# Optimization experiments

Measured on AMD Instinct MI355X. Metric: run time of the kernel, lower is better.

Reference implementation:

```python
import jax, jax.numpy as jnp
import numpy as np

N = 100000      # total nodes in batched graph
E_RAND = 1600000  # random edges (avg degree 16); self-loops appended -> E = E_RAND + N
B = 1024        # number of graphs / descriptor batch
DIN, D2D, D3D = 128, 200, 100
DG, DH = 20, 64
H1, H2 = 128, 32
EPS = 1e-5


def _lin_init(key, fan_in, fan_out):
    k1, k2 = jax.random.split(key)
    bound = 1.0 / np.sqrt(fan_in)
    W = jax.random.uniform(k1, (fan_in, fan_out), jnp.float32, -bound, bound)
    b = jax.random.uniform(k2, (fan_out,), jnp.float32, -bound, bound)
    return W, b


def setup_inputs() -> dict:
    key = jax.random.key(0)
    ks = jax.random.split(key, 16)
    feat = jax.random.normal(ks[0], (N, DIN), jnp.float32)
    src_r = jax.random.randint(ks[1], (E_RAND,), 0, N, jnp.int32)
    dst_r = jax.random.randint(ks[2], (E_RAND,), 0, N, jnp.int32)
    loop = jnp.arange(N, dtype=jnp.int32)
    src = jnp.concatenate([src_r, loop])  # self-loops: every node has in-degree >= 1
    dst = jnp.concatenate([dst_r, loop])
    graph_id = ((jnp.arange(N, dtype=jnp.int64) * B) // N).astype(jnp.int32)  # sorted, all B nonempty
    desc_2d = jax.random.normal(ks[3], (B, D2D), jnp.float32)
    desc_3d = jax.random.normal(ks[4], (B, D3D), jnp.float32)
    Wg1, bg1 = _lin_init(ks[5], DIN, 100)
    Wg2, bg2 = _lin_init(ks[6], 100, DG)
    Wpg, bpg = _lin_init(ks[7], DG, DH)
    Wp2, bp2 = _lin_init(ks[8], D2D, DH)
    gain = np.sqrt(6.0 / (DH + DH))
    W2 = jax.random.uniform(ks[9], (DH, DH), jnp.float32, -gain, gain)  # xavier_uniform
    Wf1, bf1 = _lin_init(ks[10], 2 * DH, H1)
    Wf2, bf2 = _lin_init(ks[11], H1, H2)
    Wf3, bf3 = _lin_init(ks[12], H2, 1)
    return dict(feat=feat, src=src, dst=dst, graph_id=graph_id,
                desc_2d=desc_2d, desc_3d=desc_3d,
                Wg1=Wg1, bg1=bg1, Wg2=Wg2, bg2=bg2,
                Wpg=Wpg, bpg=bpg, Wp2=Wp2, bp2=bp2, W2=W2,
                Wf1=Wf1, bf1=bf1, Wf2=Wf2, bf2=bf2, Wf3=Wf3, bf3=bf3,
                bn1_g=jnp.ones((H1,), jnp.float32), bn1_b=jnp.zeros((H1,), jnp.float32),
                bn2_g=jnp.ones((H2,), jnp.float32), bn2_b=jnp.zeros((H2,), jnp.float32))


def _gcn(h, W, b, src, dst):
    # copy_u -> mailbox mean: segment-mean of source feats over destination
    msg = h[src]                                               # [E, d] gather
    s = jax.ops.segment_sum(msg, dst, num_segments=N)          # [N, d]
    deg = jax.ops.segment_sum(jnp.ones((src.shape[0], 1), h.dtype), dst, num_segments=N)
    accum = s / jnp.maximum(deg, 1.0)
    return jax.nn.relu(accum @ W + b)


def _bn(x, g, b):  # BatchNorm1d, training-mode batch stats (biased var)
    mu = jnp.mean(x, axis=0)
    var = jnp.mean(jnp.square(x - mu), axis=0)
    return g * (x - mu) * jax.lax.rsqrt(var + EPS) + b


def reference(feat, src, dst, graph_id, desc_2d, desc_3d,
              Wg1, bg1, Wg2, bg2, Wpg, bpg, Wp2, bp2, W2,
              Wf1, bf1, Wf2, bf2, Wf3, bf3, bn1_g, bn1_b, bn2_g, bn2_b):
    h = _gcn(feat, Wg1, bg1, src, dst)        # relu(GCN1) -> [N,100]
    h = _gcn(h, Wg2, bg2, src, dst)           # relu(GCN2) -> [N,20]
    # dgl.mean_nodes: per-graph mean
    hs = jax.ops.segment_sum(h, graph_id, num_segments=B)
    cnt = jax.ops.segment_sum(jnp.ones((N, 1), h.dtype), graph_id, num_segments=B)
    hg = hs / jnp.maximum(cnt, 1.0)           # [B, 20]
    h_g = hg @ Wpg + bpg                      # [B, 64]
    h_d = desc_2d @ Wp2 + bp2                 # [B, 64]
    gate_vec = jax.nn.sigmoid((h_g @ W2) * h_d)
    v2 = gate_vec * h_d
    fusion = jnp.concatenate([h_g, v2], axis=-1)   # [B, 128]
    out = jax.nn.relu(_bn(fusion @ Wf1 + bf1, bn1_g, bn1_b))
    out = jax.nn.relu(_bn(out @ Wf2 + bf2, bn2_g, bn2_b))
    return out @ Wf3 + bf3                    # [B, 1]
```

## Files before the change

kernel.cpp:

```cpp
#include <hip/hip_runtime.h>
#include <hip/hip_fp8.h>
#include <math.h>

#define N_NODES 100000
#define B_GRAPH 1024
#define NBKT 391
#define NBLK 416
#define CAP 6000

typedef unsigned short ushort_t;
typedef unsigned int uint_t;
typedef unsigned char uchar_t;
typedef __attribute__((ext_vector_type(8))) short short8v;
typedef __attribute__((ext_vector_type(4))) float f32x4;
typedef __attribute__((ext_vector_type(2))) float f32x2;

static inline size_t alignup(size_t x){ return (x + 255) & ~(size_t)255; }

__device__ inline float bflo(uint_t u){
  union{ uint_t i; float f; } v; v.i = u << 16; return v.f;
}
__device__ inline float bfhi(uint_t u){
  union{ uint_t i; float f; } v; v.i = u & 0xffff0000u; return v.f;
}
__device__ inline ushort_t f2bf(float f){
  union{ float f; uint_t i; } v; v.f = f;
  uint_t b = v.i;
  b += 0x7fffu + ((b >> 16) & 1u);
  return (ushort_t)(b >> 16);
}
__device__ inline uint_t packbf(float a, float b){
  return (uint_t)f2bf(a) | ((uint_t)f2bf(b) << 16);
}
__device__ inline uchar_t f2fp8(float f){
  __hip_fp8_e4m3 v(f); return (uchar_t)v.__x;
}

__global__ __launch_bounds__(256) void k_hist(const int* __restrict__ dst,
                                              int* __restrict__ hist_g, int* __restrict__ btot,
                                              int E, int CH){
  __shared__ int h[NBKT];
  int blk = blockIdx.x, t = threadIdx.x;
  for (int i = t; i < NBKT; i += 256) h[i] = 0;
  __syncthreads();
  int s = blk*CH, e = s + CH; if (e > E) e = E;
  for (int i = s + t; i < e; i += 256) atomicAdd(&h[dst[i] >> 8], 1);
  __syncthreads();
  for (int i = t; i < NBKT; i += 256){
    int v = h[i];
    hist_g[i*NBLK + blk] = v;
    if (v) atomicAdd(&btot[i], v);
  }
}

__global__ __launch_bounds__(512) void k_offs(const int* __restrict__ hist_g, const int* __restrict__ btot,
                                              int* __restrict__ offs, int* __restrict__ bbase){
  __shared__ int sc[512];
  int b = blockIdx.x, t = threadIdx.x;
  int acc = 0;
  for (int i = t; i < b; i += 512) acc += btot[i];
  sc[t] = acc; __syncthreads();
  for (int o = 256; o > 0; o >>= 1){ if (t < o) sc[t] += sc[t+o]; __syncthreads(); }
  int bb = sc[0];
  __syncthreads();
  int v = (t < NBLK) ? hist_g[b*NBLK + t] : 0;
  sc[t] = v; __syncthreads();
  for (int off = 1; off < 512; off <<= 1){
    int u = (t >= off) ? sc[t-off] : 0;
    __syncthreads();
    sc[t] += u;
    __syncthreads();
  }
  if (t < NBLK) offs[b*NBLK + t] = bb + sc[t] - v;
  if (t == 0) bbase[b] = bb;
  if (b == NBKT-1 && t == NBLK-1) bbase[NBKT] = bb + sc[t];
}

__global__ __launch_bounds__(256) void k_scatter(const int* __restrict__ src, const int* __restrict__ dst,
                                                 const int* __restrict__ offs, uint_t* __restrict__ pairs,
                                                 int E, int CH){
  __shared__ int base[NBKT];
  int blk = blockIdx.x, t = threadIdx.x;
  for (int i = t; i < NBKT; i += 256) base[i] = offs[i*NBLK + blk];
  __syncthreads();
  int s = blk*CH, e = s + CH; if (e > E) e = E;
  for (int i = s + t; i < e; i += 256){
    int d = dst[i];
    int pos = atomicAdd(&base[d >> 8], 1);
    pairs[pos] = (uint_t)src[i] | ((uint_t)(d & 255) << 17);
  }
}

__global__ __launch_bounds__(256) void k_final(const uint_t* __restrict__ pairs, const int* __restrict__ bbase,
                                               int* __restrict__ rp, int* __restrict__ col){
  __shared__ uint_t buf[CAP];
  __shared__ int dcnt[256];
  __shared__ int sc[256];
  __shared__ int dpos[256];
  int b = blockIdx.x, t = threadIdx.x;
  int s = bbase[b], e = bbase[b+1], n = e - s;
  dcnt[t] = 0;
  const uint_t* P;
  if (n <= CAP){
    for (int i = t; i < n; i += 256) buf[i] = pairs[s + i];
    P = buf;
  } else {
    P = pairs + s;
  }
  __syncthreads();
  for (int i = t; i < n; i += 256) atomicAdd(&dcnt[P[i] >> 17], 1);
  __syncthreads();
  int v = dcnt[t];
  sc[t] = v; __syncthreads();
  for (int off = 1; off < 256; off <<= 1){
    int u = (t >= off) ? sc[t-off] : 0;
    __syncthreads();
    sc[t] += u;
    __syncthreads();
  }
  int ex = sc[t] - v;
  int node = b*256 + t;
  if (node <= N_NODES) rp[node] = s + ex;
  dpos[t] = s + ex;
  __syncthreads();
  for (int i = t; i < n; i += 256){
    uint_t pr = P[i];
    int pos = atomicAdd(&dpos[pr >> 17], 1);
    col[pos] = (int)(pr & 0x1FFFFu);
  }
}

__global__ __launch_bounds__(256) void k_packw(const float* __restrict__ W, ushort_t* __restrict__ wpk){
  int idx = blockIdx.x*256 + threadIdx.x;
  if (idx >= 7*4*64) return;
  int l = idx & 63;
  int s = (idx >> 6) & 3;
  int ct = idx >> 8;
  int colj = ct*16 + (l & 15);
  int kbase = 32*s + ((l >> 4) << 3);
  #pragma unroll
  for (int j = 0; j < 8; j++){
    float w = (colj < 100) ? W[(kbase + j)*100 + colj] : 0.f;
    wpk[idx*8 + j] = f2bf(w);
  }
}

__global__ __launch_bounds__(256) void k_gemm1m(const float* __restrict__ feat, const ushort_t* __restrict__ wpk,
                                                uchar_t* __restrict__ t1, int Nn){
  int wid = threadIdx.x >> 6;
  int lane = threadIdx.x & 63;
  int rt = blockIdx.x*4 + wid;
  int row0 = rt*16;
  if (row0 >= Nn) return;
  short8v a[4];
  const float* arow = feat + (size_t)(row0 + (lane & 15))*128 + ((lane >> 4) << 3);
  #pragma unroll
  for (int s = 0; s < 4; s++){
    float4 f0 = *reinterpret_cast<const float4*>(arow + 32*s);
    float4 f1 = *reinterpret_cast<const float4*>(arow + 32*s + 4);
    union { short8v v; uint_t u[4]; } cv;
    cv.u[0] = packbf(f0.x, f0.y); cv.u[1] = packbf(f0.z, f0.w);
    cv.u[2] = packbf(f1.x, f1.y); cv.u[3] = packbf(f1.z, f1.w);
    a[s] = cv.v;
  }
  const short8v* bfrag = reinterpret_cast<const short8v*>(wpk);
  for (int ct = 0; ct < 7; ct++){
    f32x4 acc = {0.f, 0.f, 0.f, 0.f};
    #pragma unroll
    for (int s = 0; s < 4; s++){
      short8v b = bfrag[(ct*4 + s)*64 + lane];
      acc = __builtin_amdgcn_mfma_f32_16x16x32_bf16(a[s], b, acc, 0, 0, 0);
    }
    int colj = ct*16 + (lane & 15);
    if (colj < 100){
      uchar_t* basep = t1 + colj;
      #pragma unroll
      for (int r = 0; r < 4; r++){
        int row = row0 + ((lane >> 4) << 2) + r;
        basep[(size_t)row*128] = f2fp8(acc[r]);
      }
    }
  }
}

__global__ __launch_bounds__(256) void k_agg1(const uint2* __restrict__ t1q, const int* __restrict__ rp,
                                              const int* __restrict__ col, const float* __restrict__ bias,
                                              uint_t* __restrict__ h1u, int Nn){
  int lane = threadIdx.x & 63;
  int node = blockIdx.x*4 + (threadIdx.x >> 6);
  if (node >= Nn) return;
  int qtr = lane >> 4;
  int q   = lane & 15;
  int rs = rp[node], re = rp[node+1];
  float s0=0.f,s1=0.f,s2=0.f,s3=0.f,s4=0.f,s5=0.f,s6=0.f,s7=0.f;

#if __has_builtin(__builtin_amdgcn_cvt_pk_f32_fp8)
  #define DEC8(U) { \
    f32x2 p0 = __builtin_amdgcn_cvt_pk_f32_fp8((U).x, 0); \
    f32x2 p1 = __builtin_amdgcn_cvt_pk_f32_fp8((U).x, 1); \
    f32x2 p2 = __builtin_amdgcn_cvt_pk_f32_fp8((U).y, 0); \
    f32x2 p3 = __builtin_amdgcn_cvt_pk_f32_fp8((U).y, 1); \
    s0 += p0[0]; s1 += p0[1]; s2 += p1[0]; s3 += p1[1]; \
    s4 += p2[0]; s5 += p2[1]; s6 += p3[0]; s7 += p3[1]; }
#else
  #define F8(B) ({ __hip_fp8_e4m3 _v; _v.__x = (unsigned char)(B); (float)_v; })
  #define DEC8(U) { \
    s0 += F8((U).x); s1 += F8((U).x>>8); s2 += F8((U).x>>16); s3 += F8((U).x>>24); \
    s4 += F8((U).y); s5 += F8((U).y>>8); s6 += F8((U).y>>16); s7 += F8((U).y>>24); }
#endif

  for (int base = rs; base < re; base += 64){
    int idx = base + lane;
    int colv = col[idx < re ? idx : re-1];
    int m = re - base; if (m > 64) m = 64;
    int nq = (m - qtr + 3) >> 2;
    int j = 0;
    for (; j + 4 <= nq; j += 4){
      int c0 = __shfl(colv, 4*(j+0) + qtr);
      int c1 = __shfl(colv, 4*(j+1) + qtr);
      int c2 = __shfl(colv, 4*(j+2) + qtr);
      int c3 = __shfl(colv, 4*(j+3) + qtr);
      uint2 u0 = t1q[(size_t)c0*16 + q];
      uint2 u1 = t1q[(size_t)c1*16 + q];
      uint2 u2 = t1q[(size_t)c2*16 + q];
      uint2 u3 = t1q[(size_t)c3*16 + q];
      DEC8(u0); DEC8(u1); DEC8(u2); DEC8(u3);
    }
    for (; j < nq; j++){
      int c = __shfl(colv, 4*j + qtr);
      uint2 u = t1q[(size_t)c*16 + q];
      DEC8(u);
    }
  }
  s0 += __shfl_xor(s0, 16); s1 += __shfl_xor(s1, 16);
  s2 += __shfl_xor(s2, 16); s3 += __shfl_xor(s3, 16);
  s4 += __shfl_xor(s4, 16); s5 += __shfl_xor(s5, 16);
  s6 += __shfl_xor(s6, 16); s7 += __shfl_xor(s7, 16);
  s0 += __shfl_xor(s0, 32); s1 += __shfl_xor(s1, 32);
  s2 += __shfl_xor(s2, 32); s3 += __shfl_xor(s3, 32);
  s4 += __shfl_xor(s4, 32); s5 += __shfl_xor(s5, 32);
  s6 += __shfl_xor(s6, 32); s7 += __shfl_xor(s7, 32);

  if (lane < 13){
    float inv = 1.f/(float)(re - rs);
    float v[8] = {s0,s1,s2,s3,s4,s5,s6,s7};
    #pragma unroll
    for (int i = 0; i < 8; i++){
      int d = 8*lane + i;
      float bv = bias[d < 100 ? d : 99];
      float x = v[i]*inv + (d < 100 ? bv : 0.f);
      v[i] = x > 0.f ? x : 0.f;
    }
    uint_t p0 = packbf(v[0],v[1]), p1 = packbf(v[2],v[3]);
    uint_t p2 = packbf(v[4],v[5]), p3 = packbf(v[6],v[7]);
    uint_t* o = h1u + (size_t)node*50 + lane*4;
    if (lane < 12){
      uint4 w4; w4.x = p0; w4.y = p1; w4.z = p2; w4.w = p3;
      *reinterpret_cast<uint4*>(o) = w4;
    } else {
      uint2 w2; w2.x = p0; w2.y = p1;
      *reinterpret_cast<uint2*>(o) = w2;
    }
  }
  #undef DEC8
}

__global__ __launch_bounds__(256) void k_gemm2(const uint_t* __restrict__ h1u, const float* __restrict__ W,
                                               ushort_t* __restrict__ t2, int Nn){
  int row = blockIdx.x*256 + threadIdx.x;
  if (row >= Nn) return;
  const uint2* xb = reinterpret_cast<const uint2*>(h1u + (size_t)row*50);
  float acc[20];
  #pragma unroll
  for (int j = 0; j < 20; j++) acc[j] = 0.f;
  #pragma unroll 5
  for (int q = 0; q < 25; q++){
    uint2 u = xb[q];
    float fx = bflo(u.x), fy = bfhi(u.x), fz = bflo(u.y), fw = bfhi(u.y);
    const float* w0 = W + q*80;
    #pragma unroll
    for (int j = 0; j < 20; j++){
      float a = acc[j];
      a = fmaf(fx, w0[j],      a);
      a = fmaf(fy, w0[20 + j], a);
      a = fmaf(fz, w0[40 + j], a);
      a = fmaf(fw, w0[60 + j], a);
      acc[j] = a;
    }
  }
  uint2* o = reinterpret_cast<uint2*>(t2 + (size_t)row*20);
  #pragma unroll
  for (int j = 0; j < 5; j++){
    uint2 v; v.x = packbf(acc[4*j], acc[4*j+1]); v.y = packbf(acc[4*j+2], acc[4*j+3]);
    o[j] = v;
  }
}

__global__ __launch_bounds__(256) void k_agg2(const uint_t* __restrict__ t2u, const int* __restrict__ rp,
                                              const int* __restrict__ col, const float* __restrict__ bias,
                                              float2* __restrict__ h2, int Nn){
  int tid = threadIdx.x;
  int node = blockIdx.x*16 + (tid >> 4);
  int l16 = tid & 15;
  if (node >= Nn) return;
  int rs = rp[node], re = rp[node+1];
  int d2 = l16 < 10 ? l16 : 9;
  int grpb = (tid & 63) & ~15;
  float slo0=0.f, slo1=0.f, shi0=0.f, shi1=0.f;
  for (int base = rs; base < re; base += 16){
    int idx = base + l16;
    int colv = col[idx < re ? idx : re-1];
    int m = re - base; if (m > 16) m = 16;
    int e = 0;
    for (; e + 4 <= m; e += 4){
      int c0 = __shfl(colv, grpb+e+0), c1 = __shfl(colv, grpb+e+1);
      int c2 = __shfl(colv, grpb+e+2), c3 = __shfl(colv, grpb+e+3);
      uint_t u0 = t2u[(size_t)c0*10 + d2];
      uint_t u1 = t2u[(size_t)c1*10 + d2];
      uint_t u2 = t2u[(size_t)c2*10 + d2];
      uint_t u3 = t2u[(size_t)c3*10 + d2];
      slo0 += bflo(u0); shi0 += bfhi(u0);
      slo1 += bflo(u1); shi1 += bfhi(u1);
      slo0 += bflo(u2); shi0 += bfhi(u2);
      slo1 += bflo(u3); shi1 += bfhi(u3);
    }
    for (; e < m; e++){
      int c = __shfl(colv, grpb+e);
      uint_t u = t2u[(size_t)c*10 + d2];
      slo0 += bflo(u); shi0 += bfhi(u);
    }
  }
  if (l16 < 10){
    float inv = 1.f/(float)(re - rs);
    float vlo = (slo0 + slo1)*inv + bias[2*l16];
    float vhi = (shi0 + shi1)*inv + bias[2*l16 + 1];
    vlo = vlo > 0.f ? vlo : 0.f;
    vhi = vhi > 0.f ? vhi : 0.f;
    float2 v; v.x = vlo; v.y = vhi;
    h2[(size_t)node*10 + l16] = v;
  }
}

__global__ __launch_bounds__(256) void k_gmean(const float* __restrict__ h2, float* __restrict__ hg){
  __shared__ float red[240];
  int g = blockIdx.x;
  int t = threadIdx.x;
  int s = (int)(((long long)g      * N_NODES + B_GRAPH - 1) / B_GRAPH);
  int e = (int)(((long long)(g+1)  * N_NODES + B_GRAPH - 1) / B_GRAPH);
  if (t < 240){
    int d  = t % 20;
    int r0 = t / 20;
    float acc = 0.f;
    for (int n = s + r0; n < e; n += 12) acc += h2[(size_t)n*20 + d];
    red[t] = acc;
  }
  __syncthreads();
  if (t < 20){
    float acc = 0.f;
    #pragma unroll
    for (int r = 0; r < 12; r++) acc += red[r*20 + t];
    hg[g*20 + t] = acc / (float)(e - s);
  }
}

__global__ __launch_bounds__(256) void k_headf(const float* __restrict__ hg, const float* __restrict__ Wpg,
                                               const float* __restrict__ bpg, const float* __restrict__ desc2,
                                               const float* __restrict__ Wp2, const float* __restrict__ bp2,
                                               const float* __restrict__ W2, float* __restrict__ fus){
  __shared__ float hGs[4][64];
  int idx = blockIdx.x*256 + threadIdx.x;
  int r = idx >> 6, d = idx & 63;
  int rloc = (threadIdx.x >> 6);
  float a = bpg[d];
  for (int k = 0; k < 20; k++) a = fmaf(hg[r*20 + k], Wpg[k*64 + d], a);
  float hd = bp2[d];
  for (int k = 0; k < 200; k++) hd = fmaf(desc2[r*200 + k], Wp2[k*64 + d], hd);
  hGs[rloc][d] = a;
  __syncthreads();
  float x = 0.f;
  for (int k = 0; k < 64; k++) x = fmaf(hGs[rloc][k], W2[k*64 + d], x);
  float gv = 1.f / (1.f + expf(-x*hd));
  fus[r*128 + d]      = a;
  fus[r*128 + 64 + d] = gv*hd;
}

__global__ __launch_bounds__(256) void k_tr(const float* __restrict__ X, float* __restrict__ XT){
  __shared__ float tile[32][33];
  int rb = blockIdx.x >> 2;
  int cb = blockIdx.x & 3;
  int tx = threadIdx.x & 31;
  int ty = threadIdx.x >> 5;
  #pragma unroll
  for (int i = 0; i < 4; i++){
    int r = rb*32 + ty + 8*i;
    tile[ty + 8*i][tx] = X[(size_t)r*128 + cb*32 + tx];
  }
  __syncthreads();
  #pragma unroll
  for (int i = 0; i < 4; i++){
    int c = cb*32 + ty + 8*i;
    XT[(size_t)c*1024 + rb*32 + tx] = tile[tx][ty + 8*i];
  }
}

__global__ __launch_bounds__(256) void k_bnt(const float* __restrict__ XT, const float* __restrict__ W,
                                             const float* __restrict__ bias, const float* __restrict__ gam,
                                             const float* __restrict__ bet, float* __restrict__ YT,
                                             int Kin, int Jout){
  int j = blockIdx.x;
  int t = threadIdx.x;
  float b0 = bias[j];
  float4 z; z.x = b0; z.y = b0; z.z = b0; z.w = b0;
  for (int k = 0; k < Kin; k++){
    float4 x = reinterpret_cast<const float4*>(XT + (size_t)k*1024)[t];
    float wv = W[k*Jout + j];
    z.x = fmaf(x.x, wv, z.x);
    z.y = fmaf(x.y, wv, z.y);
    z.z = fmaf(x.z, wv, z.z);
    z.w = fmaf(x.w, wv, z.w);
  }
  float s = z.x+z.y+z.z+z.w;
  float q = z.x*z.x+z.y*z.y+z.z*z.z+z.w*z.w;
  __shared__ float rs_[256], rq_[256];
  rs_[t] = s; rq_[t] = q; __syncthreads();
  for (int o = 128; o > 0; o >>= 1){
    if (t < o){ rs_[t] += rs_[t+o]; rq_[t] += rq_[t+o]; }
    __syncthreads();
  }
  float mu  = rs_[0] * (1.f/1024.f);
  float var = rq_[0] * (1.f/1024.f) - mu*mu;
  float inv = 1.f / sqrtf(var + 1e-5f);
  float gj = gam[j], bj = bet[j];
  float4 y;
  y.x = gj*(z.x-mu)*inv + bj; y.x = y.x > 0.f ? y.x : 0.f;
  y.y = gj*(z.y-mu)*inv + bj; y.y = y.y > 0.f ? y.y : 0.f;
  y.z = gj*(z.z-mu)*inv + bj; y.z = y.z > 0.f ? y.z : 0.f;
  y.w = gj*(z.w-mu)*inv + bj; y.w = y.w > 0.f ? y.w : 0.f;
  reinterpret_cast<float4*>(YT + (size_t)j*1024)[t] = y;
}

__global__ __launch_bounds__(256) void k_out(const float* __restrict__ y2T, const float* __restrict__ Wf3,
                                             const float* __restrict__ bf3, float* __restrict__ out){
  int r = blockIdx.x*256 + threadIdx.x;
  if (r >= B_GRAPH) return;
  float a = bf3[0];
  #pragma unroll
  for (int k = 0; k < 32; k++) a = fmaf(y2T[k*1024 + r], Wf3[k], a);
  out[r] = a;
}

extern "C" void kernel_launch(void* const* d_in, const int* in_sizes, int n_in,
                              void* d_out, int out_size, void* d_ws, size_t ws_size,
                              hipStream_t stream){
  const float* feat  = (const float*)d_in[0];
  const int*   src   = (const int*)d_in[1];
  const int*   dst   = (const int*)d_in[2];
  const float* desc2 = (const float*)d_in[4];
  const float* Wg1   = (const float*)d_in[6];
  const float* bg1   = (const float*)d_in[7];
  const float* Wg2   = (const float*)d_in[8];
  const float* bg2   = (const float*)d_in[9];
  const float* Wpg   = (const float*)d_in[10];
  const float* bpg   = (const float*)d_in[11];
  const float* Wp2   = (const float*)d_in[12];
  const float* bp2   = (const float*)d_in[13];
  const float* W2    = (const float*)d_in[14];
  const float* Wf1   = (const float*)d_in[15];
  const float* bf1   = (const float*)d_in[16];
  const float* Wf2   = (const float*)d_in[17];
  const float* bf2   = (const float*)d_in[18];
  const float* Wf3   = (const float*)d_in[19];
  const float* bf3   = (const float*)d_in[20];
  const float* bn1g  = (const float*)d_in[21];
  const float* bn1b  = (const float*)d_in[22];
  const float* bn2g  = (const float*)d_in[23];
  const float* bn2b  = (const float*)d_in[24];
  float* out = (float*)d_out;
  const int E = in_sizes[1];

  char* w = (char*)d_ws;
  int* rp     = (int*)w; w += alignup((size_t)(N_NODES+1)*4);
  int* col    = (int*)w; w += alignup((size_t)E*4);
  int* hist_g = (int*)w; w += alignup((size_t)NBKT*NBLK*4);
  int* offs   = (int*)w; w += alignup((size_t)NBKT*NBLK*4);
  int* btot   = (int*)w; w += alignup((size_t)NBKT*4);
  int* bbase  = (int*)w; w += alignup((size_t)(NBKT+1)*4);
  ushort_t* wpk = (ushort_t*)w; w += alignup((size_t)7*4*64*8*2);
  uchar_t* t1 = (uchar_t*)w; w += alignup((size_t)N_NODES*128);
  char* regionA = w; w += alignup((size_t)N_NODES*50*4);
  ushort_t* t2 = (ushort_t*)w; w += alignup((size_t)N_NODES*20*2);
  float* h2   = (float*)w; w += alignup((size_t)N_NODES*20*4);
  float* hg  = (float*)w; w += alignup((size_t)B_GRAPH*20*4);
  float* fus = (float*)w; w += alignup((size_t)B_GRAPH*128*4);
  float* fusT= (float*)w; w += alignup((size_t)B_GRAPH*128*4);
  float* y1T = (float*)w; w += alignup((size_t)B_GRAPH*128*4);
  float* y2T = (float*)w; w += alignup((size_t)B_GRAPH*32*4);
  uint_t* pairs = (uint_t*)regionA;
  uint_t* h1u   = (uint_t*)regionA;

  const int CH = (E + NBLK - 1)/NBLK;

  hipMemsetAsync(btot, 0, (size_t)NBKT*sizeof(int), stream);
  hipMemsetAsync(t1, 0, (size_t)N_NODES*128, stream);
  k_hist   <<<NBLK, 256, 0, stream>>>(dst, hist_g, btot, E, CH);
  k_offs   <<<NBKT, 512, 0, stream>>>(hist_g, btot, offs, bbase);
  k_scatter<<<NBLK, 256, 0, stream>>>(src, dst, offs, pairs, E, CH);
  k_final  <<<NBKT, 256, 0, stream>>>(pairs, bbase, rp, col);

  k_packw  <<<7, 256, 0, stream>>>(Wg1, wpk);
  k_gemm1m <<<(N_NODES/16 + 3)/4, 256, 0, stream>>>(feat, wpk, t1, N_NODES);
  k_agg1   <<<(N_NODES+3)/4, 256, 0, stream>>>((const uint2*)t1, rp, col, bg1, h1u, N_NODES);
  k_gemm2  <<<(N_NODES+255)/256, 256, 0, stream>>>(h1u, Wg2, t2, N_NODES);
  k_agg2   <<<(N_NODES+15)/16, 256, 0, stream>>>((const uint_t*)t2, rp, col, bg2, (float2*)h2, N_NODES);

  k_gmean  <<<B_GRAPH, 256, 0, stream>>>(h2, hg);
  k_headf  <<<(B_GRAPH*64)/256, 256, 0, stream>>>(hg, Wpg, bpg, desc2, Wp2, bp2, W2, fus);
  k_tr     <<<128, 256, 0, stream>>>(fus, fusT);
  k_bnt    <<<128, 256, 0, stream>>>(fusT, Wf1, bf1, bn1g, bn1b, y1T, 128, 128);
  k_bnt    <<<32, 256, 0, stream>>>(y1T, Wf2, bf2, bn2g, bn2b, y2T, 128, 32);
  k_out    <<<4, 256, 0, stream>>>(y2T, Wf3, bf3, out);
}
```

Baseline: 270.4 us.

## Fuse second GCN linear layer into first aggregation kernel via LDS

Merges k_gemm2 into the layer-1 aggregation kernel. Each wave keeps its node's aggregated 100-wide fp32 row in shared memory and does the 100x20 Wg2 product across lanes, writing bf16 t2 directly. This drops the bf16 h1 intermediate round-trip to global memory and one kernel launch. Accumulators become packed f32x2 so the fp8 decode adds can use packed adds. In exchange it adds a block barrier and a small per-wave matvec that reads Wg2 from cache, and h1 is no longer rounded to bf16.

```diff
diff --git a/kernel.cpp b/kernel.cpp
--- a/kernel.cpp
+++ b/kernel.cpp
@@ -183,30 +183,30 @@
   }
 }
 
-__global__ __launch_bounds__(256) void k_agg1(const uint2* __restrict__ t1q, const int* __restrict__ rp,
-                                              const int* __restrict__ col, const float* __restrict__ bias,
-                                              uint_t* __restrict__ h1u, int Nn){
+__global__ __launch_bounds__(256) void k_agg1f(const uint2* __restrict__ t1q, const int* __restrict__ rp,
+                                               const int* __restrict__ col, const float* __restrict__ bias,
+                                               const float* __restrict__ Wg2, ushort_t* __restrict__ t2, int Nn){
+  __shared__ float h1s[4][104];
   int lane = threadIdx.x & 63;
-  int node = blockIdx.x*4 + (threadIdx.x >> 6);
+  int w = threadIdx.x >> 6;
+  int node = blockIdx.x*4 + w;
   if (node >= Nn) return;
   int qtr = lane >> 4;
   int q   = lane & 15;
   int rs = rp[node], re = rp[node+1];
-  float s0=0.f,s1=0.f,s2=0.f,s3=0.f,s4=0.f,s5=0.f,s6=0.f,s7=0.f;
+  f32x2 a0 = {0.f,0.f}, a1 = {0.f,0.f}, a2 = {0.f,0.f}, a3 = {0.f,0.f};
 
 #if __has_builtin(__builtin_amdgcn_cvt_pk_f32_fp8)
   #define DEC8(U) { \
-    f32x2 p0 = __builtin_amdgcn_cvt_pk_f32_fp8((U).x, 0); \
-    f32x2 p1 = __builtin_amdgcn_cvt_pk_f32_fp8((U).x, 1); \
-    f32x2 p2 = __builtin_amdgcn_cvt_pk_f32_fp8((U).y, 0); \
-    f32x2 p3 = __builtin_amdgcn_cvt_pk_f32_fp8((U).y, 1); \
-    s0 += p0[0]; s1 += p0[1]; s2 += p1[0]; s3 += p1[1]; \
-    s4 += p2[0]; s5 += p2[1]; s6 += p3[0]; s7 += p3[1]; }
+    a0 += __builtin_amdgcn_cvt_pk_f32_fp8((U).x, 0); \
+    a1 += __builtin_amdgcn_cvt_pk_f32_fp8((U).x, 1); \
+    a2 += __builtin_amdgcn_cvt_pk_f32_fp8((U).y, 0); \
+    a3 += __builtin_amdgcn_cvt_pk_f32_fp8((U).y, 1); }
 #else
   #define F8(B) ({ __hip_fp8_e4m3 _v; _v.__x = (unsigned char)(B); (float)_v; })
   #define DEC8(U) { \
-    s0 += F8((U).x); s1 += F8((U).x>>8); s2 += F8((U).x>>16); s3 += F8((U).x>>24); \
-    s4 += F8((U).y); s5 += F8((U).y>>8); s6 += F8((U).y>>16); s7 += F8((U).y>>24); }
+    a0.x += F8((U).x); a0.y += F8((U).x>>8); a1.x += F8((U).x>>16); a1.y += F8((U).x>>24); \
+    a2.x += F8((U).y); a2.y += F8((U).y>>8); a3.x += F8((U).y>>16); a3.y += F8((U).y>>24); }
 #endif
 
   for (int base = rs; base < re; base += 64){
@@ -232,68 +232,39 @@
       DEC8(u);
     }
   }
-  s0 += __shfl_xor(s0, 16); s1 += __shfl_xor(s1, 16);
-  s2 += __shfl_xor(s2, 16); s3 += __shfl_xor(s3, 16);
-  s4 += __shfl_xor(s4, 16); s5 += __shfl_xor(s5, 16);
-  s6 += __shfl_xor(s6, 16); s7 += __shfl_xor(s7, 16);
-  s0 += __shfl_xor(s0, 32); s1 += __shfl_xor(s1, 32);
-  s2 += __shfl_xor(s2, 32); s3 += __shfl_xor(s3, 32);
-  s4 += __shfl_xor(s4, 32); s5 += __shfl_xor(s5, 32);
-  s6 += __shfl_xor(s6, 32); s7 += __shfl_xor(s7, 32);
+  a0.x += __shfl_xor(a0.x, 16); a0.y += __shfl_xor(a0.y, 16);
+  a1.x += __shfl_xor(a1.x, 16); a1.y += __shfl_xor(a1.y, 16);
+  a2.x += __shfl_xor(a2.x, 16); a2.y += __shfl_xor(a2.y, 16);
+  a3.x += __shfl_xor(a3.x, 16); a3.y += __shfl_xor(a3.y, 16);
+  a0.x += __shfl_xor(a0.x, 32); a0.y += __shfl_xor(a0.y, 32);
+  a1.x += __shfl_xor(a1.x, 32); a1.y += __shfl_xor(a1.y, 32);
+  a2.x += __shfl_xor(a2.x, 32); a2.y += __shfl_xor(a2.y, 32);
+  a3.x += __shfl_xor(a3.x, 32); a3.y += __shfl_xor(a3.y, 32);
 
   if (lane < 13){
     float inv = 1.f/(float)(re - rs);
-    float v[8] = {s0,s1,s2,s3,s4,s5,s6,s7};
+    float v[8] = {a0.x,a0.y,a1.x,a1.y,a2.x,a2.y,a3.x,a3.y};
     #pragma unroll
     for (int i = 0; i < 8; i++){
       int d = 8*lane + i;
-      float bv = bias[d < 100 ? d : 99];
-      float x = v[i]*inv + (d < 100 ? bv : 0.f);
-      v[i] = x > 0.f ? x : 0.f;
-    }
-    uint_t p0 = packbf(v[0],v[1]), p1 = packbf(v[2],v[3]);
-    uint_t p2 = packbf(v[4],v[5]), p3 = packbf(v[6],v[7]);
-    uint_t* o = h1u + (size_t)node*50 + lane*4;
-    if (lane < 12){
-      uint4 w4; w4.x = p0; w4.y = p1; w4.z = p2; w4.w = p3;
-      *reinterpret_cast<uint4*>(o) = w4;
-    } else {
-      uint2 w2; w2.x = p0; w2.y = p1;
-      *reinterpret_cast<uint2*>(o) = w2;
-    }
-  }
+      float bv = (d < 100) ? bias[d] : 0.f;
+      float x = v[i]*inv + bv;
+      h1s[w][8*lane + i] = x > 0.f ? x : 0.f;
+    }
+  }
+  __syncthreads();
+  int g = lane >= 60 ? 3 : lane/20;
+  int j = lane - g*20;
+  int d0 = (g == 0) ? 0 : (g == 1) ? 34 : (g == 2) ? 67 : 100;
+  int d1 = (g == 0) ? 34 : (g == 1) ? 67 : 100;
+  float p = 0.f;
+  for (int d = d0; d < d1; d++)
+    p = fmaf(h1s[w][d], Wg2[d*20 + j], p);
+  float pa = __shfl(p, lane + 20);
+  float pb = __shfl(p, lane + 40);
+  if (lane < 20)
+    t2[(size_t)node*20 + lane] = f2bf(p + pa + pb);
   #undef DEC8
-}
-
-__global__ __launch_bounds__(256) void k_gemm2(const uint_t* __restrict__ h1u, const float* __restrict__ W,
-                                               ushort_t* __restrict__ t2, int Nn){
-  int row = blockIdx.x*256 + threadIdx.x;
-  if (row >= Nn) return;
-  const uint2* xb = reinterpret_cast<const uint2*>(h1u + (size_t)row*50);
-  float acc[20];
-  #pragma unroll
-  for (int j = 0; j < 20; j++) acc[j] = 0.f;
-  #pragma unroll 5
-  for (int q = 0; q < 25; q++){
-    uint2 u = xb[q];
-    float fx = bflo(u.x), fy = bfhi(u.x), fz = bflo(u.y), fw = bfhi(u.y);
-    const float* w0 = W + q*80;
-    #pragma unroll
-    for (int j = 0; j < 20; j++){
-      float a = acc[j];
-      a = fmaf(fx, w0[j],      a);
-      a = fmaf(fy, w0[20 + j], a);
-      a = fmaf(fz, w0[40 + j], a);
-      a = fmaf(fw, w0[60 + j], a);
-      acc[j] = a;
-    }
-  }
-  uint2* o = reinterpret_cast<uint2*>(t2 + (size_t)row*20);
-  #pragma unroll
-  for (int j = 0; j < 5; j++){
-    uint2 v; v.x = packbf(acc[4*j], acc[4*j+1]); v.y = packbf(acc[4*j+2], acc[4*j+3]);
-    o[j] = v;
-  }
 }
 
 __global__ __launch_bounds__(256) void k_agg2(const uint_t* __restrict__ t2u, const int* __restrict__ rp,
@@ -487,7 +458,7 @@
   int* bbase  = (int*)w; w += alignup((size_t)(NBKT+1)*4);
   ushort_t* wpk = (ushort_t*)w; w += alignup((size_t)7*4*64*8*2);
   uchar_t* t1 = (uchar_t*)w; w += alignup((size_t)N_NODES*128);
-  char* regionA = w; w += alignup((size_t)N_NODES*50*4);
+  uint_t* pairs = (uint_t*)w; w += alignup((size_t)E*4);
   ushort_t* t2 = (ushort_t*)w; w += alignup((size_t)N_NODES*20*2);
   float* h2   = (float*)w; w += alignup((size_t)N_NODES*20*4);
   float* hg  = (float*)w; w += alignup((size_t)B_GRAPH*20*4);
@@ -495,8 +466,6 @@
   float* fusT= (float*)w; w += alignup((size_t)B_GRAPH*128*4);
   float* y1T = (float*)w; w += alignup((size_t)B_GRAPH*128*4);
   float* y2T = (float*)w; w += alignup((size_t)B_GRAPH*32*4);
-  uint_t* pairs = (uint_t*)regionA;
-  uint_t* h1u   = (uint_t*)regionA;
 
   const int CH = (E + NBLK - 1)/NBLK;
 
@@ -509,8 +478,7 @@
 
   k_packw  <<<7, 256, 0, stream>>>(Wg1, wpk);
   k_gemm1m <<<(N_NODES/16 + 3)/4, 256, 0, stream>>>(feat, wpk, t1, N_NODES);
-  k_agg1   <<<(N_NODES+3)/4, 256, 0, stream>>>((const uint2*)t1, rp, col, bg1, h1u, N_NODES);
-  k_gemm2  <<<(N_NODES+255)/256, 256, 0, stream>>>(h1u, Wg2, t2, N_NODES);
+  k_agg1f  <<<(N_NODES+3)/4, 256, 0, stream>>>((const uint2*)t1, rp, col, bg1, Wg2, t2, N_NODES);
   k_agg2   <<<(N_NODES+15)/16, 256, 0, stream>>>((const uint_t*)t2, rp, col, bg2, (float2*)h2, N_NODES);
 
   k_gmean  <<<B_GRAPH, 256, 0, stream>>>(h2, hg);
```

Result: slower. 316.4 us (+17.0%).
